# Performance work log

Measured on AMD Instinct MI355X. Metric: run time of the kernel, lower is better.

Reference implementation:

```python
import jax, jax.numpy as jnp
import numpy as np

D_MODEL = 1024
NUM_HEADS = 16
HEAD_DIM = D_MODEL // NUM_HEADS
B, S = 4, 2048


def setup_inputs() -> dict:
    key = jax.random.key(0)
    ks = jax.random.split(key, 12)
    scale = 1.0 / np.sqrt(D_MODEL)
    inp = {
        "query": jax.random.normal(ks[0], (B, S, D_MODEL), jnp.float32),
        "key": jax.random.normal(ks[1], (B, S, D_MODEL), jnp.float32),
        "value": jax.random.normal(ks[2], (B, S, D_MODEL), jnp.float32),
        "mask": jax.random.randint(ks[3], (1, 1, S, S), 0, 2, jnp.int32),
        "Wq": jax.random.normal(ks[4], (D_MODEL, D_MODEL), jnp.float32) * scale,
        "bq": jnp.zeros((D_MODEL,), jnp.float32),
        "Wk": jax.random.normal(ks[5], (D_MODEL, D_MODEL), jnp.float32) * scale,
        "bk": jnp.zeros((D_MODEL,), jnp.float32),
        "Wv": jax.random.normal(ks[6], (D_MODEL, D_MODEL), jnp.float32) * scale,
        "bv": jnp.zeros((D_MODEL,), jnp.float32),
        "Wo": jax.random.normal(ks[7], (D_MODEL, D_MODEL), jnp.float32) * scale,
        "bo": jnp.zeros((D_MODEL,), jnp.float32),
    }
    return inp


def reference(query, key, value, mask, Wq, bq, Wk, bk, Wv, bv, Wo, bo):
    b = query.shape[0]
    # torch nn.Linear: x @ W.T + b
    Q = query @ Wq.T + bq
    K = key @ Wk.T + bk
    V = value @ Wv.T + bv
    # [B, S, H, Dh] -> [B, H, S, Dh]
    Q = Q.reshape(b, -1, NUM_HEADS, HEAD_DIM).transpose(0, 2, 1, 3)
    K = K.reshape(b, -1, NUM_HEADS, HEAD_DIM).transpose(0, 2, 1, 3)
    V = V.reshape(b, -1, NUM_HEADS, HEAD_DIM).transpose(0, 2, 1, 3)
    # scores [B, H, Sq, Sk]
    energy = jnp.einsum("bhqd,bhkd->bhqk", Q, K) / np.sqrt(HEAD_DIM).astype(np.float32)
    energy = jnp.where(mask == 0, jnp.float32(-1e20), energy)
    attention = jax.nn.softmax(energy, axis=-1)
    x = jnp.einsum("bhqk,bhkd->bhqd", attention, V)
    x = x.transpose(0, 2, 1, 3).reshape(b, -1, D_MODEL)
    return x @ Wo.T + bo
```

## Files before the change

### kernel.cpp

```cpp
#include <hip/hip_runtime.h>
#include <hip/hip_bf16.h>

typedef __attribute__((ext_vector_type(8))) short bf16x8;
typedef __attribute__((ext_vector_type(4))) short bf16x4;
typedef __attribute__((ext_vector_type(4))) float f32x4;
typedef __attribute__((ext_vector_type(16))) float f32x16;

#define GLOBAL_AS __attribute__((address_space(1)))
#define LDS_AS __attribute__((address_space(3)))

static __device__ __forceinline__ void async16(void* lds, const void* g) {
  __builtin_amdgcn_global_load_lds((const GLOBAL_AS void*)g, (LDS_AS void*)lds, 16, 0, 0);
}

static __device__ __forceinline__ short f2bf(float f) {
  union { float f; unsigned u; } v; v.f = f;
  unsigned r = v.u + 0x7fffu + ((v.u >> 16) & 1u);
  return (short)(r >> 16);
}

static __device__ __forceinline__ unsigned cvtpk(float lo, float hi) {
  unsigned r;
  asm("v_cvt_pk_bf16_f32 %0, %1, %2" : "=v"(r) : "v"(lo), "v"(hi));
  return r;
}

#define EXP2(x) __builtin_amdgcn_exp2f(x)

#define S_LEN 2048
#define D_MODEL 1024
#define H_DIM 64
#define M_TOT 8192
#define QSCALE 0.18033688011112042f

__global__ __launch_bounds__(256) void convert_pack(
    const float* __restrict__ q, const float* __restrict__ k, const float* __restrict__ v,
    const float* __restrict__ wq, const float* __restrict__ wk, const float* __restrict__ wv,
    const float* __restrict__ wo, const int* __restrict__ mask,
    short* __restrict__ qb, short* __restrict__ kb, short* __restrict__ vb,
    short* __restrict__ wqb, short* __restrict__ wkb, short* __restrict__ wvb,
    short* __restrict__ wob, unsigned long long* __restrict__ mbits)
{
  int bid = blockIdx.x;
  if (bid < 14336) {
    long long e = ((long long)bid * 256 + threadIdx.x) * 8;
    const float* src; short* dst; long long off;
    if      (e < 8388608)  { src = q;  dst = qb;  off = e; }
    else if (e < 16777216) { src = k;  dst = kb;  off = e - 8388608; }
    else if (e < 25165824) { src = v;  dst = vb;  off = e - 16777216; }
    else if (e < 26214400) { src = wq; dst = wqb; off = e - 25165824; }
    else if (e < 27262976) { src = wk; dst = wkb; off = e - 26214400; }
    else if (e < 28311552) { src = wv; dst = wvb; off = e - 27262976; }
    else                   { src = wo; dst = wob; off = e - 28311552; }
    float4 f0 = *(const float4*)(src + off);
    float4 f1 = *(const float4*)(src + off + 4);
    bf16x8 r;
    r[0]=f2bf(f0.x); r[1]=f2bf(f0.y); r[2]=f2bf(f0.z); r[3]=f2bf(f0.w);
    r[4]=f2bf(f1.x); r[5]=f2bf(f1.y); r[6]=f2bf(f1.z); r[7]=f2bf(f1.w);
    *(bf16x8*)(dst + off) = r;
  } else {
    int wid = (bid - 14336) * 4 + (threadIdx.x >> 6);
    int lane = threadIdx.x & 63;
    int mv = mask[(long long)wid * 64 + lane];
    unsigned long long bal = __ballot(mv != 0);
    if (lane == 0) mbits[wid] = bal;
  }
}

struct GB { const short* A; const short* Bt; void* C; const float* bias; float scale; int N; int mode; };

template<int OUT_BF16>
__global__ __launch_bounds__(256) void gemm_bt(GB g0, GB g1, GB g2)
{
  GB g = (blockIdx.z == 0) ? g0 : ((blockIdx.z == 1) ? g1 : g2);
  const int K = 1024;
  const int N = g.N;
  __shared__ __align__(16) short As[128 * 32];
  __shared__ __align__(16) short Bs[128 * 32];
  int tid = threadIdx.x;
  int lane = tid & 63, wave = tid >> 6;
  int wr = wave >> 1, wc = wave & 1;
  int bx = blockIdx.x, by = blockIdx.y;
  if (g.mode & 4) { int flat = by * 8 + bx; bx = flat & 63; by = flat >> 6; }
  long long m0 = (long long)by * 128;
  int n0 = bx * 128;
  const short* Ab = g.A + m0 * K;
  const short* Bb = g.Bt + (long long)n0 * K;

  f32x4 acc[4][4];
#pragma unroll
  for (int m = 0; m < 4; ++m)
#pragma unroll
    for (int n = 0; n < 4; ++n) { f32x4 z = {0.f,0.f,0.f,0.f}; acc[m][n] = z; }

  for (int k0 = 0; k0 < K; k0 += 32) {
    __syncthreads();
#pragma unroll
    for (int it = 0; it < 2; ++it) {
      int f = it * 256 + tid;
      int row = f >> 2, cs = f & 3, c = cs ^ (row & 3);
      async16(&As[(it * 256 + (tid & 192)) * 8], Ab + (long long)row * K + k0 + c * 8);
    }
#pragma unroll
    for (int it = 0; it < 2; ++it) {
      int f = it * 256 + tid;
      int row = f >> 2, cs = f & 3, c = cs ^ (row & 3);
      async16(&Bs[(it * 256 + (tid & 192)) * 8], Bb + (long long)row * K + k0 + c * 8);
    }
    __syncthreads();

    bf16x8 af[4], bfr[4];
#pragma unroll
    for (int m = 0; m < 4; ++m) {
      int r = wr * 64 + m * 16 + (lane & 15);
      int cs = (lane >> 4) ^ (r & 3);
      af[m] = *(const bf16x8*)&As[r * 32 + cs * 8];
    }
#pragma unroll
    for (int n = 0; n < 4; ++n) {
      int r = wc * 64 + n * 16 + (lane & 15);
      int cs = (lane >> 4) ^ (r & 3);
      bfr[n] = *(const bf16x8*)&Bs[r * 32 + cs * 8];
    }
#pragma unroll
    for (int m = 0; m < 4; ++m)
#pragma unroll
      for (int n = 0; n < 4; ++n)
        acc[m][n] = __builtin_amdgcn_mfma_f32_16x16x32_bf16(af[m], bfr[n], acc[m][n], 0, 0, 0);
  }

  int cc = lane & 15;
  if (g.mode & 2) cc = (cc & 3) | ((cc & 4) << 1) | ((cc & 8) >> 1);
  bool brow_mode = (g.mode & 1) != 0;
  float bcol[4];
  if (!brow_mode) {
#pragma unroll
    for (int n = 0; n < 4; ++n) bcol[n] = g.bias[n0 + wc * 64 + n * 16 + (lane & 15)];
  }
  long long crow0 = m0 + wr * 64 + ((lane >> 4) * 4);
  int ccol0 = n0 + wc * 64 + cc;
#pragma unroll
  for (int m = 0; m < 4; ++m) {
    float brow[4];
    if (brow_mode) {
#pragma unroll
      for (int j = 0; j < 4; ++j) brow[j] = g.bias[crow0 + m * 16 + j];
    }
#pragma unroll
    for (int n = 0; n < 4; ++n)
#pragma unroll
      for (int j = 0; j < 4; ++j) {
        long long row = crow0 + m * 16 + j;
        int col = ccol0 + n * 16;
        float val = (acc[m][n][j] + (brow_mode ? brow[j] : bcol[n])) * g.scale;
        if (OUT_BF16) ((short*)g.C)[row * N + col] = f2bf(val);
        else          ((float*)g.C)[row * N + col] = val;
      }
  }
}

__global__ __launch_bounds__(256, 3) void attn_fwd(
    const short* __restrict__ Qb, const short* __restrict__ Kb, const short* __restrict__ Vtg,
    const unsigned long long* __restrict__ mbits, short* __restrict__ Xb)
{
  int bh = blockIdx.y;
  int b = bh >> 4, hh = bh & 15;
  int q0 = blockIdx.x * 128;
  int tid = threadIdx.x, lane = tid & 63, wave = tid >> 6;
  int ql = lane & 31, h = lane >> 5;
  const short* Qh = Qb + (long long)b * S_LEN * D_MODEL + hh * H_DIM;
  const short* Kh = Kb + (long long)b * S_LEN * D_MODEL + hh * H_DIM;
  const short* Vh = Vtg + (long long)(hh * H_DIM) * M_TOT + b * S_LEN;

  __shared__ __align__(16) short Ks[2][64 * 64];
  __shared__ __align__(16) short Vs[2][64 * 64];

  int qr = q0 + wave * 32 + ql;
  bf16x8 qf[4];
#pragma unroll
  for (int dk = 0; dk < 4; ++dk)
    qf[dk] = *(const bf16x8*)&Qh[(long long)qr * D_MODEL + dk * 16 + h * 8];

  const int fA = tid, fB = 256 + tid;
  const int rA = fA >> 3, rB = fB >> 3;
  const int swA = ((fA & 7) ^ (rA & 7)) * 8, swB = ((fB & 7) ^ (rB & 7)) * 8;
  const int kgA = rA * D_MODEL + swA, kgB = rB * D_MODEL + swB;
  const int vgA = rA * M_TOT + swA,  vgB = rB * M_TOT + swB;
  const int ldA = (tid & 192) * 8, ldB = (256 + (tid & 192)) * 8;

  int rdK[2][4];
#pragma unroll
  for (int kt = 0; kt < 2; ++kt)
#pragma unroll
    for (int dk = 0; dk < 4; ++dk)
      rdK[kt][dk] = (kt * 32 + ql) * 64 + (((2 * dk + h) ^ (lane & 7)) * 8);
  int rdV[2][4];
#pragma unroll
  for (int dt = 0; dt < 2; ++dt)
#pragma unroll
    for (int kt16 = 0; kt16 < 4; ++kt16)
      rdV[dt][kt16] = (dt * 32 + ql) * 64 + (((2 * kt16 + h) ^ (lane & 7)) * 8);

  const unsigned long long* mpb = mbits + (long long)qr * 32;

  f32x16 accO[2], INIT;
#pragma unroll
  for (int r = 0; r < 16; ++r) { accO[0][r] = 0.f; accO[1][r] = 0.f; INIT[r] = -4.0f; }
  float lrow = 0.f;

#define STAGE(t, BUF) do {                                                   \
    const short* Kt_ = Kh + (long long)(t) * (64 * D_MODEL);                 \
    async16(&Ks[BUF][ldA], Kt_ + kgA);                                       \
    async16(&Ks[BUF][ldB], Kt_ + kgB);                                       \
    const short* Vt_ = Vh + (t) * 64;                                        \
    async16(&Vs[BUF][ldA], Vt_ + vgA);                                       \
    async16(&Vs[BUF][ldB], Vt_ + vgB);                                       \
  } while (0)

#define TILE(t, CUR) do {                                                            \
    unsigned long long mw_next = ((t) < 31) ? mpb[(t) + 1] : 0ull;                   \
    if ((t) < 31) STAGE((t) + 1, 1 - (CUR));                                         \
    const short* ksb = &Ks[CUR][0];                                                  \
    const short* vsb = &Vs[CUR][0];                                                  \
    unsigned long long msh = mw >> (4 * h);                                          \
    bf16x8 pbf[4];                                                                   \
    _Pragma("unroll") for (int kt = 0; kt < 2; ++kt) {                               \
      bf16x8 kf0 = *(const bf16x8*)(ksb + rdK[kt][0]);                               \
      f32x16 s = __builtin_amdgcn_mfma_f32_32x32x16_bf16(kf0, qf[0], INIT, 0, 0, 0); \
      _Pragma("unroll") for (int dk = 1; dk < 4; ++dk) {                             \
        bf16x8 kf = *(const bf16x8*)(ksb + rdK[kt][dk]);                             \
        s = __builtin_amdgcn_mfma_f32_32x32x16_bf16(kf, qf[dk], s, 0, 0, 0);         \
      }                                                                              \
      unsigned mwd = kt ? (unsigned)(msh >> 32) : (unsigned)msh;                     \
      float pe[16];                                                                  \
      _Pragma("unroll") for (int r = 0; r < 16; ++r) {                               \
        float pv = EXP2(s[r]);                                                       \
        int sm = __builtin_amdgcn_sbfe(mwd, (r & 3) + 8 * (r >> 2), 1);              \
        union { float f; unsigned u; } pu; pu.f = pv;                                \
        pu.u &= (unsigned)sm;                                                        \
        pe[r] = pu.f;                                                                \
      }                                                                              \
      float s0_ = pe[0] + pe[1],   s1_ = pe[2] + pe[3];                              \
      float s2_ = pe[4] + pe[5],   s3_ = pe[6] + pe[7];                              \
      float s4_ = pe[8] + pe[9],   s5_ = pe[10] + pe[11];                            \
      float s6_ = pe[12] + pe[13], s7_ = pe[14] + pe[15];                            \
      lrow += ((s0_ + s1_) + (s2_ + s3_)) + ((s4_ + s5_) + (s6_ + s7_));             \
      union { unsigned w[4]; bf16x8 v; } b0, b1;                                     \
      b0.w[0] = cvtpk(pe[0], pe[1]);   b0.w[1] = cvtpk(pe[2], pe[3]);                \
      b0.w[2] = cvtpk(pe[4], pe[5]);   b0.w[3] = cvtpk(pe[6], pe[7]);                \
      b1.w[0] = cvtpk(pe[8], pe[9]);   b1.w[1] = cvtpk(pe[10], pe[11]);              \
      b1.w[2] = cvtpk(pe[12], pe[13]); b1.w[3] = cvtpk(pe[14], pe[15]);              \
      pbf[kt * 2] = b0.v; pbf[kt * 2 + 1] = b1.v;                                    \
    }                                                                                \
    __builtin_amdgcn_s_setprio(1);                                                   \
    _Pragma("unroll") for (int kt16 = 0; kt16 < 4; ++kt16) {                         \
      _Pragma("unroll") for (int dt = 0; dt < 2; ++dt) {                             \
        bf16x8 vf = *(const bf16x8*)(vsb + rdV[dt][kt16]);                           \
        accO[dt] = __builtin_amdgcn_mfma_f32_32x32x16_bf16(vf, pbf[kt16], accO[dt], 0, 0, 0); \
      }                                                                              \
    }                                                                                \
    __builtin_amdgcn_s_setprio(0);                                                   \
    mw = mw_next;                                                                    \
    __syncthreads();         \
  } while (0)

  STAGE(0, 0);
  unsigned long long mw = mpb[0];
  __syncthreads();

  for (int t = 0; t < 32; t += 2) {
    TILE(t, 0);
    TILE(t + 1, 1);
  }

  lrow += __shfl_xor(lrow, 32);
  float inv = 1.0f / lrow;

  short* xb = Xb + ((long long)b * S_LEN + qr) * D_MODEL + hh * H_DIM;
#pragma unroll
  for (int dt = 0; dt < 2; ++dt)
#pragma unroll
    for (int r0 = 0; r0 < 16; r0 += 4) {
      int d0 = dt * 32 + 8 * (r0 >> 2) + 4 * h;
      union { unsigned w[2]; bf16x4 v; } ob;
      ob.w[0] = cvtpk(accO[dt][r0 + 0] * inv, accO[dt][r0 + 1] * inv);
      ob.w[1] = cvtpk(accO[dt][r0 + 2] * inv, accO[dt][r0 + 3] * inv);
      *(bf16x4*)&xb[d0] = ob.v;
    }
#undef TILE
#undef STAGE
}

extern "C" void kernel_launch(void* const* d_in, const int* in_sizes, int n_in,
                              void* d_out, int out_size, void* d_ws, size_t ws_size,
                              hipStream_t stream) {
  const float* q   = (const float*)d_in[0];
  const float* k   = (const float*)d_in[1];
  const float* v   = (const float*)d_in[2];
  const int*  mask = (const int*)d_in[3];
  const float* Wq  = (const float*)d_in[4];
  const float* bq  = (const float*)d_in[5];
  const float* Wk  = (const float*)d_in[6];
  const float* bk  = (const float*)d_in[7];
  const float* Wv  = (const float*)d_in[8];
  const float* bv  = (const float*)d_in[9];
  const float* Wo  = (const float*)d_in[10];
  const float* bo  = (const float*)d_in[11];

  char* w = (char*)d_ws;
  short* qb  = (short*)(w + 0LL);
  short* kb  = (short*)(w + 16777216LL);
  short* vb  = (short*)(w + 33554432LL);
  short* wqb = (short*)(w + 50331648LL);
  short* wkb = (short*)(w + 52428800LL);
  short* wvb = (short*)(w + 54525952LL);
  short* wob = (short*)(w + 56623104LL);
  short* Qb  = (short*)(w + 58720256LL);
  short* Kb  = (short*)(w + 75497472LL);
  short* Vtg = (short*)(w + 92274688LL);
  short* Xb  = (short*)(w + 109051904LL);
  unsigned long long* mbits = (unsigned long long*)(w + 125829120LL);

  convert_pack<<<30720, 256, 0, stream>>>(q, k, v, Wq, Wk, Wv, Wo, mask,
                                          qb, kb, vb, wqb, wkb, wvb, wob, mbits);
  GB gq{qb, wqb, (void*)Qb, bq, QSCALE, 1024, 0};
  GB gk{kb, wkb, (void*)Kb, bk, 1.0f, 1024, 0};
  GB gv{wvb, vb, (void*)Vtg, bv, 1.0f, 8192, 1 | 2 | 4};
  gemm_bt<1><<<dim3(8, 64, 3), 256, 0, stream>>>(gq, gk, gv);

  attn_fwd<<<dim3(16, 64), 256, 0, stream>>>(Qb, Kb, Vtg, mbits, Xb);

  GB go{Xb, wob, d_out, bo, 1.0f, 1024, 0};
  gemm_bt<0><<<dim3(8, 64, 1), 256, 0, stream>>>(go, go, go);
}
```

Baseline: 230.9 us.

## Fuse fp32-to-bf16 activation conversion into projection GEMM tile loads

Drops the separate conversion pass over the q/k/v activations. The projection GEMMs now load fp32 tiles into LDS with a wider swizzle and convert them to bf16 at fragment-read time using packed convert instructions. This removes a full read and write of the activations through HBM. The cost is double LDS footprint and load count for the fp32 operand, extra conversion ALU work in the inner loop, and splitting the V projection into its own launch without the block remapping it had before.

Measured after the change: 263.1 us. 14.0% more time.

```diff
diff --git a/kernel.cpp b/kernel.cpp
--- a/kernel.cpp
+++ b/kernel.cpp
@@ -34,24 +34,19 @@
 #define QSCALE 0.18033688011112042f
 
 __global__ __launch_bounds__(256) void convert_pack(
-    const float* __restrict__ q, const float* __restrict__ k, const float* __restrict__ v,
     const float* __restrict__ wq, const float* __restrict__ wk, const float* __restrict__ wv,
     const float* __restrict__ wo, const int* __restrict__ mask,
-    short* __restrict__ qb, short* __restrict__ kb, short* __restrict__ vb,
     short* __restrict__ wqb, short* __restrict__ wkb, short* __restrict__ wvb,
     short* __restrict__ wob, unsigned long long* __restrict__ mbits)
 {
   int bid = blockIdx.x;
-  if (bid < 14336) {
+  if (bid < 2048) {
     long long e = ((long long)bid * 256 + threadIdx.x) * 8;
     const float* src; short* dst; long long off;
-    if      (e < 8388608)  { src = q;  dst = qb;  off = e; }
-    else if (e < 16777216) { src = k;  dst = kb;  off = e - 8388608; }
-    else if (e < 25165824) { src = v;  dst = vb;  off = e - 16777216; }
-    else if (e < 26214400) { src = wq; dst = wqb; off = e - 25165824; }
-    else if (e < 27262976) { src = wk; dst = wkb; off = e - 26214400; }
-    else if (e < 28311552) { src = wv; dst = wvb; off = e - 27262976; }
-    else                   { src = wo; dst = wob; off = e - 28311552; }
+    if      (e < 1048576) { src = wq; dst = wqb; off = e; }
+    else if (e < 2097152) { src = wk; dst = wkb; off = e - 1048576; }
+    else if (e < 3145728) { src = wv; dst = wvb; off = e - 2097152; }
+    else                  { src = wo; dst = wob; off = e - 3145728; }
     float4 f0 = *(const float4*)(src + off);
     float4 f1 = *(const float4*)(src + off + 4);
     bf16x8 r;
@@ -59,7 +54,7 @@
     r[4]=f2bf(f1.x); r[5]=f2bf(f1.y); r[6]=f2bf(f1.z); r[7]=f2bf(f1.w);
     *(bf16x8*)(dst + off) = r;
   } else {
-    int wid = (bid - 14336) * 4 + (threadIdx.x >> 6);
+    int wid = (bid - 2048) * 4 + (threadIdx.x >> 6);
     int lane = threadIdx.x & 63;
     int mv = mask[(long long)wid * 64 + lane];
     unsigned long long bal = __ballot(mv != 0);
@@ -69,23 +64,21 @@
 
 struct GB { const short* A; const short* Bt; void* C; const float* bias; float scale; int N; int mode; };
 
-template<int OUT_BF16>
+template<int OUT_BF16, int A32, int B32>
 __global__ __launch_bounds__(256) void gemm_bt(GB g0, GB g1, GB g2)
 {
   GB g = (blockIdx.z == 0) ? g0 : ((blockIdx.z == 1) ? g1 : g2);
   const int K = 1024;
   const int N = g.N;
-  __shared__ __align__(16) short As[128 * 32];
-  __shared__ __align__(16) short Bs[128 * 32];
+  __shared__ __align__(16) short As[128 * 32 * (A32 ? 2 : 1)];
+  __shared__ __align__(16) short Bs[128 * 32 * (B32 ? 2 : 1)];
   int tid = threadIdx.x;
   int lane = tid & 63, wave = tid >> 6;
   int wr = wave >> 1, wc = wave & 1;
-  int bx = blockIdx.x, by = blockIdx.y;
-  if (g.mode & 4) { int flat = by * 8 + bx; bx = flat & 63; by = flat >> 6; }
-  long long m0 = (long long)by * 128;
-  int n0 = bx * 128;
-  const short* Ab = g.A + m0 * K;
-  const short* Bb = g.Bt + (long long)n0 * K;
+  long long m0 = (long long)blockIdx.y * 128;
+  int n0 = blockIdx.x * 128;
+  const short* Ab = g.A + (A32 ? 2 : 1) * m0 * K;
+  const short* Bb = g.Bt + (B32 ? 2 : 1) * (long long)n0 * K;
 
   f32x4 acc[4][4];
 #pragma unroll
@@ -95,32 +88,77 @@
 
   for (int k0 = 0; k0 < K; k0 += 32) {
     __syncthreads();
-#pragma unroll
-    for (int it = 0; it < 2; ++it) {
-      int f = it * 256 + tid;
-      int row = f >> 2, cs = f & 3, c = cs ^ (row & 3);
-      async16(&As[(it * 256 + (tid & 192)) * 8], Ab + (long long)row * K + k0 + c * 8);
-    }
-#pragma unroll
-    for (int it = 0; it < 2; ++it) {
-      int f = it * 256 + tid;
-      int row = f >> 2, cs = f & 3, c = cs ^ (row & 3);
-      async16(&Bs[(it * 256 + (tid & 192)) * 8], Bb + (long long)row * K + k0 + c * 8);
+    if (A32) {
+      const float* Af = (const float*)Ab;
+#pragma unroll
+      for (int it = 0; it < 4; ++it) {
+        int f = it * 256 + tid;
+        int row = f >> 3, cs = f & 7, c = cs ^ (row & 7);
+        async16(&((float*)As)[(it * 256 + (tid & 192)) * 4],
+                Af + (long long)row * K + k0 + c * 4);
+      }
+    } else {
+#pragma unroll
+      for (int it = 0; it < 2; ++it) {
+        int f = it * 256 + tid;
+        int row = f >> 2, cs = f & 3, c = cs ^ (row & 3);
+        async16(&As[(it * 256 + (tid & 192)) * 8], Ab + (long long)row * K + k0 + c * 8);
+      }
+    }
+    if (B32) {
+      const float* Bf = (const float*)Bb;
+#pragma unroll
+      for (int it = 0; it < 4; ++it) {
+        int f = it * 256 + tid;
+        int row = f >> 3, cs = f & 7, c = cs ^ (row & 7);
+        async16(&((float*)Bs)[(it * 256 + (tid & 192)) * 4],
+                Bf + (long long)row * K + k0 + c * 4);
+      }
+    } else {
+#pragma unroll
+      for (int it = 0; it < 2; ++it) {
+        int f = it * 256 + tid;
+        int row = f >> 2, cs = f & 3, c = cs ^ (row & 3);
+        async16(&Bs[(it * 256 + (tid & 192)) * 8], Bb + (long long)row * K + k0 + c * 8);
+      }
     }
     __syncthreads();
 
+    int gq = lane >> 4;
     bf16x8 af[4], bfr[4];
 #pragma unroll
     for (int m = 0; m < 4; ++m) {
       int r = wr * 64 + m * 16 + (lane & 15);
-      int cs = (lane >> 4) ^ (r & 3);
-      af[m] = *(const bf16x8*)&As[r * 32 + cs * 8];
+      if (A32) {
+        const float* Asf = (const float*)As;
+        int c0 = (2 * gq) ^ (r & 7), c1 = (2 * gq + 1) ^ (r & 7);
+        f32x4 v0 = *(const f32x4*)&Asf[(r * 8 + c0) * 4];
+        f32x4 v1 = *(const f32x4*)&Asf[(r * 8 + c1) * 4];
+        union { unsigned w[4]; bf16x8 v; } fu;
+        fu.w[0] = cvtpk(v0[0], v0[1]); fu.w[1] = cvtpk(v0[2], v0[3]);
+        fu.w[2] = cvtpk(v1[0], v1[1]); fu.w[3] = cvtpk(v1[2], v1[3]);
+        af[m] = fu.v;
+      } else {
+        int cs = gq ^ (r & 3);
+        af[m] = *(const bf16x8*)&As[r * 32 + cs * 8];
+      }
     }
 #pragma unroll
     for (int n = 0; n < 4; ++n) {
       int r = wc * 64 + n * 16 + (lane & 15);
-      int cs = (lane >> 4) ^ (r & 3);
-      bfr[n] = *(const bf16x8*)&Bs[r * 32 + cs * 8];
+      if (B32) {
+        const float* Bsf = (const float*)Bs;
+        int c0 = (2 * gq) ^ (r & 7), c1 = (2 * gq + 1) ^ (r & 7);
+        f32x4 v0 = *(const f32x4*)&Bsf[(r * 8 + c0) * 4];
+        f32x4 v1 = *(const f32x4*)&Bsf[(r * 8 + c1) * 4];
+        union { unsigned w[4]; bf16x8 v; } fu;
+        fu.w[0] = cvtpk(v0[0], v0[1]); fu.w[1] = cvtpk(v0[2], v0[3]);
+        fu.w[2] = cvtpk(v1[0], v1[1]); fu.w[3] = cvtpk(v1[2], v1[3]);
+        bfr[n] = fu.v;
+      } else {
+        int cs = gq ^ (r & 3);
+        bfr[n] = *(const bf16x8*)&Bs[r * 32 + cs * 8];
+      }
     }
 #pragma unroll
     for (int m = 0; m < 4; ++m)
@@ -308,9 +346,6 @@
   const float* bo  = (const float*)d_in[11];
 
   char* w = (char*)d_ws;
-  short* qb  = (short*)(w + 0LL);
-  short* kb  = (short*)(w + 16777216LL);
-  short* vb  = (short*)(w + 33554432LL);
   short* wqb = (short*)(w + 50331648LL);
   short* wkb = (short*)(w + 52428800LL);
   short* wvb = (short*)(w + 54525952LL);
@@ -321,15 +356,16 @@
   short* Xb  = (short*)(w + 109051904LL);
   unsigned long long* mbits = (unsigned long long*)(w + 125829120LL);
 
-  convert_pack<<<30720, 256, 0, stream>>>(q, k, v, Wq, Wk, Wv, Wo, mask,
-                                          qb, kb, vb, wqb, wkb, wvb, wob, mbits);
-  GB gq{qb, wqb, (void*)Qb, bq, QSCALE, 1024, 0};
-  GB gk{kb, wkb, (void*)Kb, bk, 1.0f, 1024, 0};
-  GB gv{wvb, vb, (void*)Vtg, bv, 1.0f, 8192, 1 | 2 | 4};
-  gemm_bt<1><<<dim3(8, 64, 3), 256, 0, stream>>>(gq, gk, gv);
+  convert_pack<<<18432, 256, 0, stream>>>(Wq, Wk, Wv, Wo, mask,
+                                          wqb, wkb, wvb, wob, mbits);
+  GB gq{(const short*)q, wqb, (void*)Qb, bq, QSCALE, 1024, 0};
+  GB gk{(const short*)k, wkb, (void*)Kb, bk, 1.0f, 1024, 0};
+  gemm_bt<1, 1, 0><<<dim3(8, 64, 2), 256, 0, stream>>>(gq, gk, gk);
+  GB gv{wvb, (const short*)v, (void*)Vtg, bv, 1.0f, 8192, 1 | 2};
+  gemm_bt<1, 0, 1><<<dim3(64, 8, 1), 256, 0, stream>>>(gv, gv, gv);
 
   attn_fwd<<<dim3(16, 64), 256, 0, stream>>>(Qb, Kb, Vtg, mbits, Xb);
 
   GB go{Xb, wob, d_out, bo, 1.0f, 1024, 0};
-  gemm_bt<0><<<dim3(8, 64, 1), 256, 0, stream>>>(go, go, go);
-}
+  gemm_bt<0, 0, 0><<<dim3(8, 64, 1), 256, 0, stream>>>(go, go, go);
+}
```
